# Kernel optimization log

Measured on AMD Instinct MI355X. Metric: run time of the kernel, lower is better.

## Reference

```python
import jax, jax.numpy as jnp
import numpy as np

# dims
B, FIN, FOUT = 4, 64, 32
FMID = min(FIN, FOUT)          # fmiddle
NCLS, NH = 4, 64               # num_classes, SPADE nhidden
S = 32                         # D = H = W
EPS = 1e-5


def conv3d(x, w, b=None, pad=1):
    # x: [N,C,D,H,W], w: [O,I,kd,kh,kw]
    out = jax.lax.conv_general_dilated(
        x, w, window_strides=(1, 1, 1), padding=[(pad, pad)] * 3,
        dimension_numbers=('NCDHW', 'OIDHW', 'NCDHW'))
    if b is not None:
        out = out + b[None, :, None, None, None]
    return out


def instance_norm(x):
    # per-sample, per-channel over spatial dims (InstanceNorm3d, affine=False)
    mu = x.mean(axis=(2, 3, 4), keepdims=True)
    var = x.var(axis=(2, 3, 4), keepdims=True)
    return (x - mu) * jax.lax.rsqrt(var + EPS)


def spade(x, y, Ws, Bs, Wg, Bg, Wb, Bb):
    # x: [B,C,D,H,W]; param stacks have leading num_classes dim; y routes per sample.
    normalized = instance_norm(x)
    ws, bs, wg, bg, wb, bb = Ws[y], Bs[y], Wg[y], Bg[y], Wb[y], Bb[y]

    def one(xi, wsi, bsi, wgi, bgi, wbi, bbi):
        xi = xi[None]  # [1,C,D,H,W]
        actv = jax.nn.relu(conv3d(xi, wsi, bsi))
        gamma = conv3d(actv, wgi, bgi)[0]
        beta = conv3d(actv, wbi, bbi)[0]
        return gamma, beta

    gamma, beta = jax.vmap(one)(x, ws, bs, wg, bg, wb, bb)
    return normalized * (1.0 + gamma) + beta


def _lrelu(t):
    return jax.nn.leaky_relu(t, 0.2)


def setup_inputs() -> dict:
    key = jax.random.key(0)
    ks = jax.random.split(key, 24)
    sc = 0.05
    inp = {
        'x': jax.random.normal(ks[0], (B, FIN, S, S, S), jnp.float32),
        'y': jax.random.randint(ks[1], (B,), 0, NCLS, jnp.int64
                                if jax.config.jax_enable_x64 else jnp.int32),
        # SPADE norm_0 stacks: label_nc = norm_nc = FIN
        's0_ws': jax.random.normal(ks[2], (NCLS, NH, FIN, 3, 3, 3), jnp.float32) * sc,
        's0_bs': jnp.zeros((NCLS, NH), jnp.float32),
        's0_wg': jax.random.normal(ks[3], (NCLS, FIN, NH, 3, 3, 3), jnp.float32) * sc,
        's0_bg': jnp.zeros((NCLS, FIN), jnp.float32),
        's0_wb': jax.random.normal(ks[4], (NCLS, FIN, NH, 3, 3, 3), jnp.float32) * sc,
        's0_bb': jnp.zeros((NCLS, FIN), jnp.float32),
        # SPADE norm_1 stacks: label_nc = norm_nc = FMID
        's1_ws': jax.random.normal(ks[5], (NCLS, NH, FMID, 3, 3, 3), jnp.float32) * sc,
        's1_bs': jnp.zeros((NCLS, NH), jnp.float32),
        's1_wg': jax.random.normal(ks[6], (NCLS, FMID, NH, 3, 3, 3), jnp.float32) * sc,
        's1_bg': jnp.zeros((NCLS, FMID), jnp.float32),
        's1_wb': jax.random.normal(ks[7], (NCLS, FMID, NH, 3, 3, 3), jnp.float32) * sc,
        's1_bb': jnp.zeros((NCLS, FMID), jnp.float32),
        # resnet convs
        'conv0_w': jax.random.normal(ks[8], (FMID, FIN, 3, 3, 3), jnp.float32) * sc,
        'conv0_b': jnp.zeros((FMID,), jnp.float32),
        'conv1_w': jax.random.normal(ks[9], (FOUT, FMID, 3, 3, 3), jnp.float32) * sc,
        'conv1_b': jnp.zeros((FOUT,), jnp.float32),
        'convs_w': jax.random.normal(ks[10], (FOUT, FIN, 1, 1, 1), jnp.float32) * sc,
    }
    return inp


def reference(x, y, s0_ws, s0_bs, s0_wg, s0_bg, s0_wb, s0_bb,
              s1_ws, s1_bs, s1_wg, s1_bg, s1_wb, s1_bb,
              conv0_w, conv0_b, conv1_w, conv1_b, convs_w):
    x_s = conv3d(x, convs_w, None, pad=0)  # learned shortcut (fin != fout, no bias)
    dx = conv3d(_lrelu(spade(x, y, s0_ws, s0_bs, s0_wg, s0_bg, s0_wb, s0_bb)),
                conv0_w, conv0_b)
    dx = conv3d(_lrelu(spade(dx, y, s1_ws, s1_bs, s1_wg, s1_bg, s1_wb, s1_bb)),
                conv1_w, conv1_b)
    return x_s + dx
```

## Files before the change

### kernel.cpp

```cpp
#include <hip/hip_runtime.h>


#define S3 32768
constexpr float EPS = 1e-5f;

typedef __attribute__((ext_vector_type(8))) short s16x8;
typedef __attribute__((ext_vector_type(4))) float f32x4;
typedef __attribute__((ext_vector_type(16))) float f32x16;
typedef __attribute__((ext_vector_type(4))) unsigned short u16x4;
typedef __attribute__((ext_vector_type(8))) unsigned short u16x8;

#define GLL(g, l)                                                        \
  __builtin_amdgcn_global_load_lds(                                      \
      (const __attribute__((address_space(1))) void*)(g),                \
      (__attribute__((address_space(3))) void*)(l), 16, 0, 0)

__device__ __forceinline__ float bf2f(unsigned short u) {
  union { unsigned int i; float f; } v; v.i = ((unsigned int)u) << 16; return v.f;
}
__device__ __forceinline__ unsigned short f2bf(float f) {
  union { float f; unsigned int i; } v; v.f = f;
  unsigned int r = (v.i + 0x7FFFu + ((v.i >> 16) & 1u)) >> 16;
  return (unsigned short)r;
}

__global__ __launch_bounds__(256) void stats_kernel(const float* __restrict__ x,
                                                    float* __restrict__ mu,
                                                    float* __restrict__ rstd) {
  const int bc = blockIdx.x;
  const float* p = x + (size_t)bc * S3;
  float s = 0.f, s2 = 0.f;
  for (int i = threadIdx.x; i < S3 / 4; i += 256) {
    float4 v = reinterpret_cast<const float4*>(p)[i];
    s  += v.x + v.y + v.z + v.w;
    s2 += v.x * v.x + v.y * v.y + v.z * v.z + v.w * v.w;
  }
  for (int off = 32; off; off >>= 1) {
    s  += __shfl_down(s, off, 64);
    s2 += __shfl_down(s2, off, 64);
  }
  __shared__ float ls[4], ls2[4];
  const int wid = threadIdx.x >> 6;
  if ((threadIdx.x & 63) == 0) { ls[wid] = s; ls2[wid] = s2; }
  __syncthreads();
  if (threadIdx.x == 0) {
    float S = 0.f, S2 = 0.f;
    for (int i = 0; i < 4; ++i) { S += ls[i]; S2 += ls2[i]; }
    const float m = S / (float)S3;
    const float var = S2 / (float)S3 - m * m;
    mu[bc] = m;
    rstd[bc] = rsqrtf(var + EPS);
  }
}

__global__ __launch_bounds__(256) void stats_t32_p1(const short* __restrict__ t,
                                                    float* __restrict__ part) {
  const int b = blockIdx.y;
  const int chunk = blockIdx.x;
  const int tid = threadIdx.x;
  const int pq = tid & 3;
  float s[8], s2[8];
#pragma unroll
  for (int j = 0; j < 8; ++j) { s[j] = 0.f; s2[j] = 0.f; }
  const int vbase = chunk * 512;
#pragma unroll
  for (int v = tid >> 2; v < 512; v += 64) {
    u16x8 u = *reinterpret_cast<const u16x8*>(
        &t[((size_t)b * S3 + vbase + v) * 32 + pq * 8]);
#pragma unroll
    for (int j = 0; j < 8; ++j) { float f = bf2f(u[j]); s[j] += f; s2[j] += f * f; }
  }
#pragma unroll
  for (int off = 4; off < 64; off <<= 1) {
#pragma unroll
    for (int j = 0; j < 8; ++j) {
      s[j]  += __shfl_xor(s[j], off, 64);
      s2[j] += __shfl_xor(s2[j], off, 64);
    }
  }
  __shared__ float red[4][4][16];
  const int wv = tid >> 6, lane = tid & 63;
  if (lane < 4) {
#pragma unroll
    for (int j = 0; j < 8; ++j) { red[wv][lane][j] = s[j]; red[wv][lane][8 + j] = s2[j]; }
  }
  __syncthreads();
  if (tid < 32) {
    const int p = tid >> 3, j = tid & 7;
    float S = 0.f, S2 = 0.f;
#pragma unroll
    for (int w = 0; w < 4; ++w) { S += red[w][p][j]; S2 += red[w][p][8 + j]; }
    const int c = p * 8 + j;
    part[((size_t)(b * 64 + chunk)) * 64 + c] = S;
    part[((size_t)(b * 64 + chunk)) * 64 + 32 + c] = S2;
  }
}

__global__ __launch_bounds__(128) void stats_t32_p2(const float* __restrict__ part,
                                                    float* __restrict__ mu,
                                                    float* __restrict__ rstd) {
  const int tid = threadIdx.x;
  const int b = tid >> 5, c = tid & 31;
  float S = 0.f, S2 = 0.f;
#pragma unroll 4
  for (int k = 0; k < 64; ++k) {
    S  += part[((size_t)(b * 64 + k)) * 64 + c];
    S2 += part[((size_t)(b * 64 + k)) * 64 + 32 + c];
  }
  const float m = S / (float)S3;
  const float var = S2 / (float)S3 - m * m;
  mu[b * 32 + c] = m;
  rstd[b * 32 + c] = rsqrtf(var + EPS);
}

__global__ __launch_bounds__(256) void transpose_x(const float* __restrict__ x,
                                                   short* __restrict__ xt) {
  const int b = blockIdx.y;
  const int v0 = blockIdx.x * 64;
  __shared__ unsigned short t[64][72];
  const int vox = threadIdx.x & 63;
  const int cg = threadIdx.x >> 6;
#pragma unroll
  for (int k = 0; k < 16; ++k) {
    const int ci = cg * 16 + k;
    t[vox][ci] = f2bf(x[((size_t)(b * 64 + ci)) * S3 + v0 + vox]);
  }
  __syncthreads();
  const int vv = threadIdx.x >> 2, part = threadIdx.x & 3;
  uint4 u0 = *reinterpret_cast<const uint4*>(&t[vv][part * 16]);
  uint4 u1 = *reinterpret_cast<const uint4*>(&t[vv][part * 16 + 8]);
  short* dst = &xt[((size_t)(b * S3 + v0 + vv)) * 64 + part * 16];
  *reinterpret_cast<uint4*>(dst) = u0;
  *reinterpret_cast<uint4*>(dst + 8) = u1;
}

__global__ __launch_bounds__(256) void repack_w(
    const float* __restrict__ wA, const float* __restrict__ wB,
    short* __restrict__ dst, const int* __restrict__ y,
    int CBLK, int CO2, int CI, long clsA, long clsB, int paired, int total) {
  const int b = blockIdx.y;
  const int idx = blockIdx.x * 256 + threadIdx.x;
  if (idx >= total) return;
  const int cls = y[b];
  const int KCH = CI / 16;
  const int ci = idx & 15;
  const int co = (idx >> 4) % CO2;
  const int rest = idx / (16 * CO2);
  const int k16 = rest % KCH;
  const int tap = rest / KCH;
  const int srcch = k16 * 16 + ci;
  float v;
  if (paired) {
    const int H = CBLK >> 1;
    const int blk = co / CBLK, w = co % CBLK;
    if (w < H)
      v = wA[(size_t)clsA * cls + ((size_t)(blk * H + w) * CI + srcch) * 27 + tap];
    else
      v = wB[(size_t)clsB * cls + ((size_t)(blk * H + w - H) * CI + srcch) * 27 + tap];
  } else {
    v = wA[(size_t)clsA * cls + ((size_t)co * CI + srcch) * 27 + tap];
  }
  dst[(((size_t)(b * 27 + tap) * KCH + k16) * CO2 + co) * 16 + ci] = (short)f2bf(v);
}

template <int CIN, int CBLK, int COTOT, int EPI, int NNORM>
__global__ __launch_bounds__(256, 2) void conv_mfma(
    const short* __restrict__ xt,
    const short* __restrict__ W,
    const float* __restrict__ bias,
    int bias_stride,
    const int* __restrict__ y,
    const short* __restrict__ xnb,
    const float* __restrict__ mu,
    const float* __restrict__ rstd,
    const float* __restrict__ bgs,
    const float* __restrict__ bbs,
    const short* __restrict__ zp,
    float* __restrict__ outf,
    short* __restrict__ outb) {
  constexpr int KCH = CIN / 16;
  constexpr int NCOG = CBLK / 32;
  constexpr int PG = 604;
  constexpr int XG = 2 * PG;
  constexpr int WG = 9 * NCOG * 64;

  __shared__ short ldsX[2][XG * 8];
  __shared__ short ldsW[2][WG * 8];

  const int tid = threadIdx.x;
  const int lane = tid & 63, wid = tid >> 6;
  const int l31 = lane & 31, khf = lane >> 5;
  const int b = blockIdx.y;
  const int cls = y[b];
  const int co_base = blockIdx.z * CBLK;
  const int tile = blockIdx.x;
  const int d0 = (tile >> 4) * 4, h0 = ((tile >> 2) & 3) * 8, w0 = (tile & 3) * 8;

  const short* gsrc[5];
#pragma unroll
  for (int k = 0; k < 5; ++k) {
    const int i = tid + k * 256;
    const short* g = zp;
    if (i < XG) {
      const int pl = (i >= PG) ? 1 : 0;
      const int slot = i - pl * PG;
      if (slot < 600) {
        const int sd = slot / 100, r0 = slot - sd * 100;
        const int sh = r0 / 10, sw0 = r0 - sh * 10;
        const int gd = d0 + sd - 1, gh = h0 + sh - 1, gw = w0 + sw0 - 1;
        if ((unsigned)gd < 32u && (unsigned)gh < 32u && (unsigned)gw < 32u)
          g = xt + ((size_t)b * S3 + gd * 1024 + gh * 32 + gw) * CIN + pl * 8;
      }
    }
    gsrc[k] = g;
  }

  auto stage_x = [&](int kc, int xb) {
#pragma unroll
    for (int k = 0; k < 5; ++k) {
      const int i = tid + k * 256;
      if (i < XG) GLL(gsrc[k] + kc * 16, &ldsX[xb][i * 8]);
    }
  };
  auto stage_w = [&](int kc, int kd, int wb) {
#pragma unroll
    for (int k = 0; k < (WG + 255) / 256; ++k) {
      const int i = tid + k * 256;
      if (i < WG) {
        const int t9 = i / (NCOG * 64);
        const int r = i - t9 * (NCOG * 64);
        const int c = r >> 6, q = r & 63;
        GLL(W + (((size_t)(b * 27 + kd * 9 + t9) * KCH + kc) * COTOT +
                 co_base + c * 32 + (q & 31)) * 16 + (q >> 5) * 8,
            &ldsW[wb][i * 8]);
      }
    }
  };

  f32x16 acc[2][NCOG];
#pragma unroll
  for (int v = 0; v < 2; ++v)
#pragma unroll
    for (int c = 0; c < NCOG; ++c)
#pragma unroll
      for (int r = 0; r < 16; ++r) acc[v][c][r] = 0.f;

  const int hw10 = (l31 >> 3) * 10 + (l31 & 7);
  const int xpl = khf * PG;

  stage_x(0, 0);
  stage_w(0, 0, 0);
  __syncthreads();

  int xb = 0;
#pragma unroll
  for (int ph = 0; ph < KCH * 3; ++ph) {
    const int kd = ph % 3;
    const int wb = ph & 1;
    if (ph + 1 < KCH * 3) {
      const int nkc = (ph + 1) / 3, nkd = (ph + 1) % 3;
      stage_w(nkc, nkd, wb ^ 1);
      if (nkd == 0) stage_x(nkc, xb ^ 1);
    }
    __builtin_amdgcn_s_setprio(1);
#pragma unroll
    for (int kh = 0; kh < 3; ++kh) {
#pragma unroll
      for (int kw = 0; kw < 3; ++kw) {
        const int t9 = kh * 3 + kw;
        s16x8 af[NCOG];
#pragma unroll
        for (int c = 0; c < NCOG; ++c)
          af[c] = *reinterpret_cast<const s16x8*>(
              &ldsW[wb][((t9 * NCOG + c) * 64 + lane) * 8]);
        s16x8 bf[2];
#pragma unroll
        for (int vg = 0; vg < 2; ++vg) {
          const int slot = (wid + kd) * 100 + (vg * 4 + kh) * 10 + kw + hw10;
          bf[vg] = *reinterpret_cast<const s16x8*>(&ldsX[xb][(xpl + slot) * 8]);
        }
#pragma unroll
        for (int c = 0; c < NCOG; ++c)
#pragma unroll
          for (int vg = 0; vg < 2; ++vg)
            acc[vg][c] = __builtin_amdgcn_mfma_f32_32x32x16_bf16(
                af[c], bf[vg], acc[vg][c], 0, 0, 0);
      }
    }
    __builtin_amdgcn_s_setprio(0);
    __syncthreads();
    if (kd == 2) xb ^= 1;
  }

  const int dgv = (d0 + wid) * 1024 + (h0 + (l31 >> 3)) * 32 + w0 + (l31 & 7);

  if constexpr (EPI == 0 || EPI == 1) {
#pragma unroll
    for (int c = 0; c < NCOG; ++c)
#pragma unroll
      for (int q = 0; q < 4; ++q) {
        const int c0 = co_base + c * 32 + q * 8 + khf * 4;
        const f32x4 b4 = *reinterpret_cast<const f32x4*>(&bias[cls * bias_stride + c0]);
#pragma unroll
        for (int vg = 0; vg < 2; ++vg) {
          const int gv = dgv + vg * 128;
          u16x4 o;
#pragma unroll
          for (int rr = 0; rr < 4; ++rr) {
            float v = acc[vg][c][q * 4 + rr] + b4[rr];
            if constexpr (EPI == 0) v = fmaxf(v, 0.f);
            o[rr] = f2bf(v);
          }
          *reinterpret_cast<u16x4*>(&outb[((size_t)b * S3 + gv) * COTOT + c0]) = o;
        }
      }
  }

  if constexpr (EPI == 2) {
    const int nb = blockIdx.z * 32;
#pragma unroll
    for (int q = 0; q < 4; ++q) {
      const int c0 = nb + q * 8 + khf * 4;
      const f32x4 m4  = *reinterpret_cast<const f32x4*>(&mu[b * NNORM + c0]);
      const f32x4 r4  = *reinterpret_cast<const f32x4*>(&rstd[b * NNORM + c0]);
      const f32x4 g4  = *reinterpret_cast<const f32x4*>(&bgs[cls * NNORM + c0]);
      const f32x4 bb4 = *reinterpret_cast<const f32x4*>(&bbs[cls * NNORM + c0]);
#pragma unroll
      for (int vg = 0; vg < 2; ++vg) {
        const int gv = dgv + vg * 128;
        const size_t vgl = (size_t)b * S3 + gv;
        u16x4 u = *reinterpret_cast<const u16x4*>(&xnb[vgl * NNORM + c0]);
        u16x4 o;
#pragma unroll
        for (int rr = 0; rr < 4; ++rr) {
          const float gamma = acc[vg][0][q * 4 + rr] + g4[rr];
          const float beta  = acc[vg][1][q * 4 + rr] + bb4[rr];
          const float nrm = (bf2f(u[rr]) - m4[rr]) * r4[rr];
          float h = nrm * (1.f + gamma) + beta;
          h = h > 0.f ? h : 0.2f * h;
          o[rr] = f2bf(h);
        }
        *reinterpret_cast<u16x4*>(&outb[vgl * NNORM + c0]) = o;
      }
    }
  }

  if constexpr (EPI == 4) {
#pragma unroll
    for (int q = 0; q < 4; ++q) {
      const int c0 = q * 8 + khf * 4;
      const f32x4 b4 = *reinterpret_cast<const f32x4*>(&bias[c0]);
#pragma unroll
      for (int vg = 0; vg < 2; ++vg) {
        const int gv = dgv + vg * 128;
#pragma unroll
        for (int rr = 0; rr < 4; ++rr) {
          float* p = &outf[((size_t)(b * 32 + c0 + rr)) * S3 + gv];
          *p += acc[vg][0][q * 4 + rr] + b4[rr];
        }
      }
    }
  }
}

__global__ __launch_bounds__(256) void shortcut_kernel(const float* __restrict__ x,
                                                       const float* __restrict__ wsc,
                                                       float* __restrict__ out) {
  const int b = blockIdx.y;
  const int v = blockIdx.x * 256 + threadIdx.x;
  __shared__ float lw[64 * 32];
  for (int i = threadIdx.x; i < 2048; i += 256) {
    int ci = i >> 5, o = i & 31;
    lw[i] = wsc[o * 64 + ci];
  }
  __syncthreads();
  float acc[32];
#pragma unroll
  for (int o = 0; o < 32; ++o) acc[o] = 0.f;
  const float* xp = x + (size_t)b * 64 * S3 + v;
#pragma unroll 1
  for (int ci = 0; ci < 64; ++ci) {
    const float xv = xp[(size_t)ci * S3];
    const float4* wp = reinterpret_cast<const float4*>(&lw[ci << 5]);
#pragma unroll
    for (int o4 = 0; o4 < 8; ++o4) {
      float4 w4 = wp[o4];
      acc[o4 * 4 + 0] += xv * w4.x;
      acc[o4 * 4 + 1] += xv * w4.y;
      acc[o4 * 4 + 2] += xv * w4.z;
      acc[o4 * 4 + 3] += xv * w4.w;
    }
  }
  float* op = out + (size_t)b * 32 * S3 + v;
#pragma unroll
  for (int o = 0; o < 32; ++o) op[(size_t)o * S3] = acc[o];
}

extern "C" void kernel_launch(void* const* d_in, const int* in_sizes, int n_in,
                              void* d_out, int out_size, void* d_ws, size_t ws_size,
                              hipStream_t stream) {
  const float* x       = (const float*)d_in[0];
  const int*   y       = (const int*)d_in[1];
  const float* s0_ws   = (const float*)d_in[2];
  const float* s0_bs   = (const float*)d_in[3];
  const float* s0_wg   = (const float*)d_in[4];
  const float* s0_bg   = (const float*)d_in[5];
  const float* s0_wb   = (const float*)d_in[6];
  const float* s0_bb   = (const float*)d_in[7];
  const float* s1_ws   = (const float*)d_in[8];
  const float* s1_bs   = (const float*)d_in[9];
  const float* s1_wg   = (const float*)d_in[10];
  const float* s1_bg   = (const float*)d_in[11];
  const float* s1_wb   = (const float*)d_in[12];
  const float* s1_bb   = (const float*)d_in[13];
  const float* conv0_w = (const float*)d_in[14];
  const float* conv0_b = (const float*)d_in[15];
  const float* conv1_w = (const float*)d_in[16];
  const float* conv1_b = (const float*)d_in[17];
  const float* convs_w = (const float*)d_in[18];

  float* out = (float*)d_out;
  char* ws = (char*)d_ws;
  short* xt    = (short*)(ws);
  short* actvT = (short*)(ws + 16777216);
  short* hT    = (short*)(ws + 33554432);
  short* d0T   = (short*)(ws + 50331648);
  short* Wa0   = (short*)(ws + 58720256);
  short* Ws0   = (short*)(ws + 60817408);
  short* Wc0   = (short*)(ws + 62914560);
  short* Wa1   = (short*)(ws + 65011712);
  short* Ws1   = (short*)(ws + 67108864);
  short* Wc1   = (short*)(ws + 69206016);
  short* zp    = (short*)(ws + 70254592);
  float* stats = (float*)(ws + 71303168);
  float* mu0 = stats, *rstd0 = stats + 256, *mu1 = stats + 512, *rstd1 = stats + 640;
  float* spart = stats + 1024;

  hipMemsetAsync(zp, 0, 4096, stream);

  transpose_x<<<dim3(512, 4), 256, 0, stream>>>(x, xt);
  stats_kernel<<<dim3(256), 256, 0, stream>>>(x, mu0, rstd0);

  repack_w<<<dim3(432, 4), 256, 0, stream>>>(s0_ws, nullptr, Wa0, y, 64, 64, 64,
                                             64L * 64 * 27, 0, 0, 110592);
  repack_w<<<dim3(864, 4), 256, 0, stream>>>(s0_wg, s0_wb, Ws0, y, 64, 128, 64,
                                             64L * 64 * 27, 64L * 64 * 27, 1, 221184);
  repack_w<<<dim3(216, 4), 256, 0, stream>>>(conv0_w, nullptr, Wc0, y, 32, 32, 64,
                                             0, 0, 0, 55296);
  repack_w<<<dim3(216, 4), 256, 0, stream>>>(s1_ws, nullptr, Wa1, y, 64, 64, 32,
                                             64L * 32 * 27, 0, 0, 55296);
  repack_w<<<dim3(432, 4), 256, 0, stream>>>(s1_wg, s1_wb, Ws1, y, 64, 64, 64,
                                             32L * 64 * 27, 32L * 64 * 27, 1, 110592);
  repack_w<<<dim3(108, 4), 256, 0, stream>>>(conv1_w, nullptr, Wc1, y, 32, 32, 32,
                                             0, 0, 0, 27648);

  conv_mfma<64, 64, 64, 0, 0><<<dim3(128, 4, 1), 256, 0, stream>>>(
      xt, Wa0, s0_bs, 64, y, nullptr, nullptr, nullptr, nullptr, nullptr, zp,
      nullptr, actvT);
  conv_mfma<64, 64, 128, 2, 64><<<dim3(128, 4, 2), 256, 0, stream>>>(
      actvT, Ws0, nullptr, 0, y, xt, mu0, rstd0, s0_bg, s0_bb, zp,
      nullptr, hT);
  conv_mfma<64, 32, 32, 1, 0><<<dim3(128, 4, 1), 256, 0, stream>>>(
      hT, Wc0, conv0_b, 0, y, nullptr, nullptr, nullptr, nullptr, nullptr, zp,
      nullptr, d0T);
  stats_t32_p1<<<dim3(64, 4), 256, 0, stream>>>(d0T, spart);
  stats_t32_p2<<<dim3(1), 128, 0, stream>>>(spart, mu1, rstd1);
  conv_mfma<32, 64, 64, 0, 0><<<dim3(128, 4, 1), 256, 0, stream>>>(
      d0T, Wa1, s1_bs, 64, y, nullptr, nullptr, nullptr, nullptr, nullptr, zp,
      nullptr, actvT);
  conv_mfma<64, 64, 64, 2, 32><<<dim3(128, 4, 1), 256, 0, stream>>>(
      actvT, Ws1, nullptr, 0, y, d0T, mu1, rstd1, s1_bg, s1_bb, zp,
      nullptr, hT);
  shortcut_kernel<<<dim3(128, 4), 256, 0, stream>>>(x, convs_w, out);
  conv_mfma<32, 32, 32, 4, 0><<<dim3(128, 4, 1), 256, 0, stream>>>(
      hT, Wc1, conv1_b, 0, y, nullptr, nullptr, nullptr, nullptr, nullptr, zp,
      out, nullptr);
}
```

Before: 287.7 us.

## Load conv weights directly from global into registers, drop LDS weight staging

Removes the double-buffered LDS staging of weight fragments and instead has each wave load its MFMA A-operands straight from global memory into registers, 9 taps at a time per kd. Only the activation tile remains LDS-staged, and barriers drop from one per (kc,kd) phase to one per kc. This frees LDS and cuts sync count, but every wave now issues redundant global weight loads and holds 9*NCOG fragments in registers, risking higher register pressure and exposed global latency before the MFMAs.

```diff
diff --git a/kernel.cpp b/kernel.cpp
--- a/kernel.cpp
+++ b/kernel.cpp
@@ -182,10 +182,8 @@
   constexpr int NCOG = CBLK / 32;
   constexpr int PG = 604;
   constexpr int XG = 2 * PG;
-  constexpr int WG = 9 * NCOG * 64;
 
   __shared__ short ldsX[2][XG * 8];
-  __shared__ short ldsW[2][WG * 8];
 
   const int tid = threadIdx.x;
   const int lane = tid & 63, wid = tid >> 6;
@@ -215,25 +213,11 @@
     gsrc[k] = g;
   }
 
-  auto stage_x = [&](int kc, int xb) {
+  auto stage_x = [&](int kc, int xbuf) {
 #pragma unroll
     for (int k = 0; k < 5; ++k) {
       const int i = tid + k * 256;
-      if (i < XG) GLL(gsrc[k] + kc * 16, &ldsX[xb][i * 8]);
-    }
-  };
-  auto stage_w = [&](int kc, int kd, int wb) {
-#pragma unroll
-    for (int k = 0; k < (WG + 255) / 256; ++k) {
-      const int i = tid + k * 256;
-      if (i < WG) {
-        const int t9 = i / (NCOG * 64);
-        const int r = i - t9 * (NCOG * 64);
-        const int c = r >> 6, q = r & 63;
-        GLL(W + (((size_t)(b * 27 + kd * 9 + t9) * KCH + kc) * COTOT +
-                 co_base + c * 32 + (q & 31)) * 16 + (q >> 5) * 8,
-            &ldsW[wb][i * 8]);
-      }
+      if (i < XG) GLL(gsrc[k] + kc * 16, &ldsX[xbuf][i * 8]);
     }
   };
 
@@ -247,49 +231,50 @@
 
   const int hw10 = (l31 >> 3) * 10 + (l31 & 7);
   const int xpl = khf * PG;
+  const int wlane = (co_base + l31) * 16 + khf * 8;
 
   stage_x(0, 0);
-  stage_w(0, 0, 0);
   __syncthreads();
 
   int xb = 0;
 #pragma unroll
-  for (int ph = 0; ph < KCH * 3; ++ph) {
-    const int kd = ph % 3;
-    const int wb = ph & 1;
-    if (ph + 1 < KCH * 3) {
-      const int nkc = (ph + 1) / 3, nkd = (ph + 1) % 3;
-      stage_w(nkc, nkd, wb ^ 1);
-      if (nkd == 0) stage_x(nkc, xb ^ 1);
-    }
-    __builtin_amdgcn_s_setprio(1);
-#pragma unroll
-    for (int kh = 0; kh < 3; ++kh) {
-#pragma unroll
-      for (int kw = 0; kw < 3; ++kw) {
-        const int t9 = kh * 3 + kw;
-        s16x8 af[NCOG];
+  for (int kc = 0; kc < KCH; ++kc) {
+#pragma unroll
+    for (int kd = 0; kd < 3; ++kd) {
+      s16x8 af[9][NCOG];
+#pragma unroll
+      for (int t9 = 0; t9 < 9; ++t9)
 #pragma unroll
         for (int c = 0; c < NCOG; ++c)
-          af[c] = *reinterpret_cast<const s16x8*>(
-              &ldsW[wb][((t9 * NCOG + c) * 64 + lane) * 8]);
-        s16x8 bf[2];
-#pragma unroll
-        for (int vg = 0; vg < 2; ++vg) {
-          const int slot = (wid + kd) * 100 + (vg * 4 + kh) * 10 + kw + hw10;
-          bf[vg] = *reinterpret_cast<const s16x8*>(&ldsX[xb][(xpl + slot) * 8]);
+          af[t9][c] = *reinterpret_cast<const s16x8*>(
+              &W[(((size_t)(b * 27 + kd * 9 + t9) * KCH + kc) * COTOT) * 16 +
+                 wlane + c * 512]);
+      if (kd == 0 && kc + 1 < KCH) stage_x(kc + 1, xb ^ 1);
+
+      __builtin_amdgcn_s_setprio(1);
+#pragma unroll
+      for (int kh = 0; kh < 3; ++kh) {
+#pragma unroll
+        for (int kw = 0; kw < 3; ++kw) {
+          const int t9 = kh * 3 + kw;
+          s16x8 bf[2];
+#pragma unroll
+          for (int vg = 0; vg < 2; ++vg) {
+            const int slot = (wid + kd) * 100 + (vg * 4 + kh) * 10 + kw + hw10;
+            bf[vg] = *reinterpret_cast<const s16x8*>(&ldsX[xb][(xpl + slot) * 8]);
+          }
+#pragma unroll
+          for (int c = 0; c < NCOG; ++c)
+#pragma unroll
+            for (int vg = 0; vg < 2; ++vg)
+              acc[vg][c] = __builtin_amdgcn_mfma_f32_32x32x16_bf16(
+                  af[t9][c], bf[vg], acc[vg][c], 0, 0, 0);
         }
-#pragma unroll
-        for (int c = 0; c < NCOG; ++c)
-#pragma unroll
-          for (int vg = 0; vg < 2; ++vg)
-            acc[vg][c] = __builtin_amdgcn_mfma_f32_32x32x16_bf16(
-                af[c], bf[vg], acc[vg][c], 0, 0, 0);
       }
-    }
-    __builtin_amdgcn_s_setprio(0);
+      __builtin_amdgcn_s_setprio(0);
+    }
     __syncthreads();
-    if (kd == 2) xb ^= 1;
+    xb ^= 1;
   }
 
   const int dgv = (d0 + wid) * 1024 + (h0 + (l31 >> 3)) * 32 + w0 + (l31 & 7);
```

After: 313.0 us. 1.09x slower.
